# Optimization experiments

Measured on AMD Instinct MI355X. Metric: run time of the kernel, lower is better.

## Reference

```python
import jax, jax.numpy as jnp
import numpy as np
import math

B, S, D, H = 8, 1024, 1024, 16
DK = D // H
DFF = 4 * D
EPS = 1e-5


def gelu_tanh(x):
    # matches the hand-written GELU: 0.5*x*(1+tanh(sqrt(2/pi)*(x+0.044715*x^3)))
    c = math.sqrt(2.0 / math.pi)
    return 0.5 * x * (1.0 + jnp.tanh(c * (x + 0.044715 * x ** 3)))


def layernorm(x, g, b):
    # faithful to the custom LayerNorm: unbiased std (ddof=1), eps added to std
    mean = jnp.mean(x, -1, keepdims=True)
    std = jnp.std(x, -1, keepdims=True, ddof=1)
    return g * (x - mean) / (std + EPS) + b


def setup_inputs() -> dict:
    key = jax.random.key(0)
    ks = jax.random.split(key, 12)
    sc_d = 1.0 / math.sqrt(D)
    sc_f = 1.0 / math.sqrt(DFF)
    inp = {
        "x": jax.random.normal(ks[0], (B, S, D), jnp.float32),
        "mask": jax.random.randint(ks[1], (B, 1, S, S), 0, 2, jnp.int32),
        "wq": jax.random.normal(ks[2], (D, D), jnp.float32) * sc_d,
        "bq": jnp.zeros((D,), jnp.float32),
        "wk": jax.random.normal(ks[3], (D, D), jnp.float32) * sc_d,
        "bk": jnp.zeros((D,), jnp.float32),
        "wv": jax.random.normal(ks[4], (D, D), jnp.float32) * sc_d,
        "bv": jnp.zeros((D,), jnp.float32),
        "wo": jax.random.normal(ks[5], (D, D), jnp.float32) * sc_d,
        "bo": jnp.zeros((D,), jnp.float32),
        "w1": jax.random.normal(ks[6], (DFF, D), jnp.float32) * sc_d,
        "b1": jnp.zeros((DFF,), jnp.float32),
        "w2": jax.random.normal(ks[7], (D, DFF), jnp.float32) * sc_f,
        "b2": jnp.zeros((D,), jnp.float32),
        "ln1_g": jnp.ones((D,), jnp.float32),
        "ln1_b": jnp.zeros((D,), jnp.float32),
        "ln2_g": jnp.ones((D,), jnp.float32),
        "ln2_b": jnp.zeros((D,), jnp.float32),
    }
    return inp


def _mha(xn, mask, wq, bq, wk, bk, wv, bv, wo, bo):
    def proj(w, b):
        y = xn @ w.T + b                       # [B,S,D]
        return y.reshape(B, S, H, DK).transpose(0, 2, 1, 3)  # [B,H,S,DK]
    q, k, v = proj(wq, bq), proj(wk, bk), proj(wv, bv)
    scores = jnp.einsum("bhqd,bhkd->bhqk", q, k) / math.sqrt(DK)
    scores = jnp.where(mask == 0, -1e9, scores)
    p = jax.nn.softmax(scores, axis=-1)
    o = jnp.einsum("bhqk,bhkd->bhqd", p, v)    # [B,H,S,DK]
    o = o.transpose(0, 2, 1, 3).reshape(B, S, D)
    return o @ wo.T + bo


def reference(x, mask, wq, bq, wk, bk, wv, bv, wo, bo, w1, b1, w2, b2,
              ln1_g, ln1_b, ln2_g, ln2_b):
    # dropout is identity in eval mode
    xn = layernorm(x, ln1_g, ln1_b)
    x = x + _mha(xn, mask, wq, bq, wk, bk, wv, bv, wo, bo)
    xn = layernorm(x, ln2_g, ln2_b)
    ff = gelu_tanh(xn @ w1.T + b1) @ w2.T + b2
    return x + ff
```

## Files before the change

kernel.cpp:

```cpp
#include <hip/hip_runtime.h>
#include <stdint.h>

typedef float f32x4 __attribute__((ext_vector_type(4)));
typedef short short8 __attribute__((ext_vector_type(8)));
typedef __bf16 bf16x8 __attribute__((ext_vector_type(8)));

static __device__ __forceinline__ short f2bf(float f) {
  unsigned u = __builtin_bit_cast(unsigned, f);
  u = (u + 0x7FFFu + ((u >> 16) & 1u)) >> 16;
  return (short)u;
}

static __device__ __forceinline__ float bf2f(short s) {
  return __builtin_bit_cast(float, (unsigned)((unsigned short)s) << 16);
}

static __device__ __forceinline__ unsigned pack2bf(float a, float b) {
  return ((unsigned)(unsigned short)f2bf(a)) |
         (((unsigned)(unsigned short)f2bf(b)) << 16);
}

static __device__ __forceinline__ f32x4 mfma16(short8 a, short8 b, f32x4 c) {
  return __builtin_amdgcn_mfma_f32_16x16x32_bf16(
      __builtin_bit_cast(bf16x8, a), __builtin_bit_cast(bf16x8, b), c, 0, 0, 0);
}

static __device__ __forceinline__ void gld_lds16(const void* g, void* s) {
  __builtin_amdgcn_global_load_lds(
      (const __attribute__((address_space(1))) void*)g,
      (__attribute__((address_space(3))) void*)s, 16, 0, 0);
}

__global__ __launch_bounds__(256) void cvt_f2bf(const float* __restrict__ in,
                                                short* __restrict__ out, int n4) {
  int i = blockIdx.x * 256 + threadIdx.x;
  if (i < n4) {
    float4 v = ((const float4*)in)[i];
    short4 o;
    o.x = f2bf(v.x); o.y = f2bf(v.y); o.z = f2bf(v.z); o.w = f2bf(v.w);
    ((short4*)out)[i] = o;
  }
}

__global__ __launch_bounds__(256) void concat3(const float* __restrict__ a,
                                               const float* __restrict__ b,
                                               const float* __restrict__ c,
                                               float* __restrict__ o) {
  int i = blockIdx.x * 256 + threadIdx.x;
  float v = (i < 1024) ? a[i] : ((i < 2048) ? b[i - 1024] : c[i - 2048]);
  o[i] = v;
}

__global__ __launch_bounds__(256) void packmask(const int* __restrict__ m,
                                                unsigned* __restrict__ out) {
  int w = blockIdx.x * 256 + threadIdx.x;
  const int4* p = (const int4*)(m + (size_t)w * 32);
  unsigned bits = 0;
#pragma unroll
  for (int c = 0; c < 8; c++) {
    int4 v = p[c];
    bits |= (unsigned)(v.x != 0) << (c * 4 + 0);
    bits |= (unsigned)(v.y != 0) << (c * 4 + 1);
    bits |= (unsigned)(v.z != 0) << (c * 4 + 2);
    bits |= (unsigned)(v.w != 0) << (c * 4 + 3);
  }
  out[w] = bits;
}

__global__ __launch_bounds__(256) void ln_bf16(const float* __restrict__ x,
                                               const float* __restrict__ g,
                                               const float* __restrict__ bb,
                                               short* __restrict__ out) {
  const int row = blockIdx.x, tid = threadIdx.x;
  const float4 xv = *(const float4*)&x[(size_t)row * 1024 + tid * 4];
  float s = xv.x + xv.y + xv.z + xv.w;
#pragma unroll
  for (int o = 32; o; o >>= 1) s += __shfl_down(s, o);
  __shared__ float red[8];
  if ((tid & 63) == 0) red[tid >> 6] = s;
  __syncthreads();
  const float mean = (red[0] + red[1] + red[2] + red[3]) * (1.f / 1024.f);
  const float a0 = xv.x - mean, a1 = xv.y - mean, a2 = xv.z - mean, a3 = xv.w - mean;
  float ss = a0 * a0 + a1 * a1 + a2 * a2 + a3 * a3;
#pragma unroll
  for (int o = 32; o; o >>= 1) ss += __shfl_down(ss, o);
  if ((tid & 63) == 0) red[4 + (tid >> 6)] = ss;
  __syncthreads();
  const float inv =
      1.f / (sqrtf((red[4] + red[5] + red[6] + red[7]) * (1.f / 1023.f)) + 1e-5f);
  const float4 gv = *(const float4*)&g[tid * 4];
  const float4 bv = *(const float4*)&bb[tid * 4];
  short4 o4;
  o4.x = f2bf(gv.x * a0 * inv + bv.x);
  o4.y = f2bf(gv.y * a1 * inv + bv.y);
  o4.z = f2bf(gv.z * a2 * inv + bv.z);
  o4.w = f2bf(gv.w * a3 * inv + bv.w);
  *(short4*)&out[(size_t)row * 1024 + tid * 4] = o4;
}

template <int ACT, int RES, int OBF>
__global__ __launch_bounds__(256) void gemm_bt(
    const short* __restrict__ A, const short* __restrict__ Bw,
    const float* __restrict__ bias, const float* __restrict__ resid,
    void* __restrict__ Cout, int M, int N, int K) {
  __shared__ alignas(1024) short As[128 * 32];
  __shared__ alignas(1024) short Bs[128 * 32];
  const int tid = threadIdx.x;
  const int l = tid & 63, w = tid >> 6;
  const int wr = w >> 1, wc = w & 1;
  const int m0 = blockIdx.y * 128, n0 = blockIdx.x * 128;
  const int fr = l & 15, fq = l >> 4;
  const size_t Ksz = (size_t)K;

  const short* ag = A + (size_t)(m0 + w * 32 + (l >> 2)) * Ksz + (l & 3) * 8;
  const short* bg = Bw + (size_t)(n0 + w * 32 + (l >> 2)) * Ksz + (l & 3) * 8;
  short* asw = As + w * 1024;
  short* bsw = Bs + w * 1024;

  f32x4 acc[4][4] = {};

  for (int kt = 0; kt < K; kt += 32) {
    gld_lds16(ag + kt, asw);
    gld_lds16(ag + kt + 16 * Ksz, asw + 512);
    gld_lds16(bg + kt, bsw);
    gld_lds16(bg + kt + 16 * Ksz, bsw + 512);
    __syncthreads();
    short8 af[4], bf[4];
#pragma unroll
    for (int m = 0; m < 4; m++)
      af[m] = *(const short8*)&As[(wr * 64 + m * 16 + fr) * 32 + fq * 8];
#pragma unroll
    for (int n = 0; n < 4; n++)
      bf[n] = *(const short8*)&Bs[(wc * 64 + n * 16 + fr) * 32 + fq * 8];
#pragma unroll
    for (int m = 0; m < 4; m++)
#pragma unroll
      for (int n = 0; n < 4; n++) acc[m][n] = mfma16(af[m], bf[n], acc[m][n]);
    __syncthreads();
  }

#pragma unroll
  for (int m = 0; m < 4; m++) {
#pragma unroll
    for (int n = 0; n < 4; n++) {
      const int row = m0 + wr * 64 + m * 16 + fq * 4;
      const int col = n0 + wc * 64 + n * 16 + fr;
      const float bvl = bias[col];
#pragma unroll
      for (int r = 0; r < 4; r++) {
        float v = acc[m][n][r] + bvl;
        if (ACT == 1) {
          float zz = 0.7978845608028654f * (v + 0.044715f * v * v * v);
          float th = 1.f - 2.f / (__expf(2.f * zz) + 1.f);
          v = 0.5f * v * (1.f + th);
        }
        if (RES) v += resid[(size_t)(row + r) * N + col];
        if (OBF)
          ((short*)Cout)[(size_t)(row + r) * N + col] = f2bf(v);
        else
          ((float*)Cout)[(size_t)(row + r) * N + col] = v;
      }
    }
  }
}

__global__ __launch_bounds__(256, 4) void attn_fwd(
    const short* __restrict__ QKV, const unsigned* __restrict__ MW,
    short* __restrict__ Om) {
  const int orig = blockIdx.x;
  const int gid = (orig & 7) * 256 + (orig >> 3);
  const int qt = gid & 15;
  const int h = (gid >> 4) & 15;
  const int b = gid >> 8;
  const int tid = threadIdx.x, l = tid & 63, w = tid >> 6;
  const int fr = l & 15, fq = l >> 4;
  __shared__ alignas(1024) short Ks[2][64 * 64];
  __shared__ alignas(1024) short Vt[2][64 * 64];
  __shared__ alignas(1024) short Ps[4][16 * 64];
  const int qbase = qt * 64;
  const size_t RS = 3072;

  short8 qf0, qf1;
  {
    const short* qp =
        QKV + ((size_t)(b * 1024 + qbase + w * 16 + fr)) * RS + h * 64 + fq * 8;
    qf0 = *(const short8*)qp;
    qf1 = *(const short8*)(qp + 32);
#pragma unroll
    for (int e = 0; e < 8; e++) {
      qf0[e] = f2bf(0.125f * bf2f(qf0[e]));
      qf1[e] = f2bf(0.125f * bf2f(qf1[e]));
    }
  }
  f32x4 m2 = {-1e30f, -1e30f, -1e30f, -1e30f};
  f32x4 lsum = {};
  f32x4 oacc[4] = {};

  const int kcol = (l & 7) ^ ((l >> 3) & 7);
  const short* kg =
      QKV + ((size_t)(b * 1024 + w * 16 + (l >> 3))) * RS + 1024 + h * 64 + kcol * 8;
  const int vkey = w * 16 + (l >> 2), vd0 = (l & 3) * 16;
  const short* vg = QKV + ((size_t)(b * 1024 + vkey)) * RS + 2048 + h * 64 + vd0;
  const int keyp = ((vkey >= 32) ? 32 : 0) + (l >> 2) * 2 + (w & 1);
  const int kslot = keyp >> 3, kbyte = keyp & 7;
  const int vxk = (l & 3) << 1;
  const unsigned* mwp = MW + ((size_t)(b * 1024 + qbase + w * 16 + fq * 4)) * 32;

  gld_lds16(kg, &Ks[0][w * 1024]);
  gld_lds16(kg + 8 * RS, &Ks[0][w * 1024 + 512]);
  short8 vv0 = *(const short8*)vg;
  short8 vv1 = *(const short8*)(vg + 8);
#pragma unroll
  for (int e = 0; e < 8; e++)
    Vt[0][(vd0 + e) * 64 + ((kslot ^ (e & 7) ^ vxk) << 3) + kbyte] = vv0[e];
#pragma unroll
  for (int e = 0; e < 8; e++)
    Vt[0][(vd0 + 8 + e) * 64 + ((kslot ^ (e & 7) ^ vxk) << 3) + kbyte] = vv1[e];
  __syncthreads();

  for (int t = 0; t < 16; t++) {
    const int cur = t & 1;
    if (t < 15) {
      const short* kgn = kg + (size_t)(t + 1) * 64 * RS;
      gld_lds16(kgn, &Ks[cur ^ 1][w * 1024]);
      gld_lds16(kgn + 8 * RS, &Ks[cur ^ 1][w * 1024 + 512]);
      const short* vgn = vg + (size_t)(t + 1) * 64 * RS;
      vv0 = *(const short8*)vgn;
      vv1 = *(const short8*)(vgn + 8);
    }
    f32x4 sv[4];
    __builtin_amdgcn_s_setprio(1);
#pragma unroll
    for (int j = 0; j < 4; j++) {
      const int row = j * 16 + fr;
      short8 k0 = *(const short8*)&Ks[cur][row * 64 + ((fq ^ (fr & 7)) << 3)];
      short8 k1 = *(const short8*)&Ks[cur][row * 64 + (((4 + fq) ^ (fr & 7)) << 3)];
      f32x4 z = {0.f, 0.f, 0.f, 0.f};
      sv[j] = mfma16(qf0, k0, z);
      sv[j] = mfma16(qf1, k1, sv[j]);
    }
    __builtin_amdgcn_s_setprio(0);
#pragma unroll
    for (int r = 0; r < 4; r++) {
      const uint2 mw = *(const uint2*)(mwp + (size_t)r * 32 + t * 2);
      float t0 = ((mw.x >> fr) & 1u) ? sv[0][r] : -3e38f;
      float t1 = ((mw.x >> (16 + fr)) & 1u) ? sv[1][r] : -3e38f;
      float t2 = ((mw.y >> fr) & 1u) ? sv[2][r] : -3e38f;
      float t3 = ((mw.y >> (16 + fr)) & 1u) ? sv[3][r] : -3e38f;
      const float pmax = fmaxf(fmaxf(t0, t1), fmaxf(t2, t3));
      if (!__all(pmax <= m2[r] + 8.f)) {
        float mx = pmax;
        mx = fmaxf(mx, __shfl_xor(mx, 1));
        mx = fmaxf(mx, __shfl_xor(mx, 2));
        mx = fmaxf(mx, __shfl_xor(mx, 4));
        mx = fmaxf(mx, __shfl_xor(mx, 8));
        const float nm = fmaxf(m2[r], mx);
        const float al = __expf(m2[r] - nm);
        m2[r] = nm;
        lsum[r] *= al;
#pragma unroll
        for (int dt = 0; dt < 4; dt++) oacc[dt][r] *= al;
      }
      const float p0 = __expf(t0 - m2[r]);
      const float p1 = __expf(t1 - m2[r]);
      const float p2 = __expf(t2 - m2[r]);
      const float p3 = __expf(t3 - m2[r]);
      lsum[r] += (p0 + p1) + (p2 + p3);
      const int q = fq * 4 + r;
      const int s0 = (fr >> 2) ^ (q & 7);
      const int s1 = (4 + (fr >> 2)) ^ (q & 7);
      *(unsigned*)&Ps[w][q * 64 + (s0 << 3) + ((fr & 3) << 1)] = pack2bf(p0, p1);
      *(unsigned*)&Ps[w][q * 64 + (s1 << 3) + ((fr & 3) << 1)] = pack2bf(p2, p3);
    }
    short8 pa0 = *(const short8*)&Ps[w][fr * 64 + ((fq ^ (fr & 7)) << 3)];
    short8 pa1 = *(const short8*)&Ps[w][fr * 64 + (((4 + fq) ^ (fr & 7)) << 3)];
    __builtin_amdgcn_s_setprio(1);
#pragma unroll
    for (int dt = 0; dt < 4; dt++) {
      const int row = dt * 16 + fr;
      const int vkx = dt << 1;
      short8 v0 = *(const short8*)&Vt[cur][row * 64 + ((fq ^ (fr & 7) ^ vkx) << 3)];
      short8 v1 =
          *(const short8*)&Vt[cur][row * 64 + (((4 + fq) ^ (fr & 7) ^ vkx) << 3)];
      oacc[dt] = mfma16(pa0, v0, oacc[dt]);
      oacc[dt] = mfma16(pa1, v1, oacc[dt]);
    }
    __builtin_amdgcn_s_setprio(0);
    if (t < 15) {
#pragma unroll
      for (int e = 0; e < 8; e++)
        Vt[cur ^ 1][(vd0 + e) * 64 + ((kslot ^ (e & 7) ^ vxk) << 3) + kbyte] = vv0[e];
#pragma unroll
      for (int e = 0; e < 8; e++)
        Vt[cur ^ 1][(vd0 + 8 + e) * 64 + ((kslot ^ (e & 7) ^ vxk) << 3) + kbyte] =
            vv1[e];
    }
    __syncthreads();
  }

#pragma unroll
  for (int r = 0; r < 4; r++) {
    float s = lsum[r];
    s += __shfl_xor(s, 1);
    s += __shfl_xor(s, 2);
    s += __shfl_xor(s, 4);
    s += __shfl_xor(s, 8);
    lsum[r] = s;
  }

#pragma unroll
  for (int dt = 0; dt < 4; dt++) {
#pragma unroll
    for (int r = 0; r < 4; r++) {
      const size_t qrow = (size_t)b * 1024 + qbase + w * 16 + fq * 4 + r;
      Om[qrow * 1024 + h * 64 + dt * 16 + fr] = f2bf(oacc[dt][r] / lsum[r]);
    }
  }
}

extern "C" void kernel_launch(void* const* d_in, const int* in_sizes, int n_in,
                              void* d_out, int out_size, void* d_ws, size_t ws_size,
                              hipStream_t stream) {
  (void)in_sizes; (void)n_in; (void)out_size; (void)ws_size;
  const float* x   = (const float*)d_in[0];
  const int*   msk = (const int*)d_in[1];
  const float* wq  = (const float*)d_in[2];
  const float* bq  = (const float*)d_in[3];
  const float* wk  = (const float*)d_in[4];
  const float* bk  = (const float*)d_in[5];
  const float* wv  = (const float*)d_in[6];
  const float* bv  = (const float*)d_in[7];
  const float* wo  = (const float*)d_in[8];
  const float* bo  = (const float*)d_in[9];
  const float* w1  = (const float*)d_in[10];
  const float* b1  = (const float*)d_in[11];
  const float* w2  = (const float*)d_in[12];
  const float* b2  = (const float*)d_in[13];
  const float* g1  = (const float*)d_in[14];
  const float* be1 = (const float*)d_in[15];
  const float* g2  = (const float*)d_in[16];
  const float* be2 = (const float*)d_in[17];
  float* out = (float*)d_out;

  char* p = (char*)d_ws;
  auto take = [&](size_t n) { char* r = p; p += (n + 1023) & ~(size_t)1023; return r; };
  const size_t MD = (size_t)8192 * 1024;
  short* XN  = (short*)take(MD * 2);
  short* BIG = (short*)take((size_t)8192 * 4096 * 2);
  short* QKV = BIG;
  short* F1  = BIG;
  short* AO  = (short*)take(MD * 2);
  float* X1  = (float*)take(MD * 4);
  unsigned* MW = (unsigned*)take((size_t)8 * 1024 * 32 * 4);
  short* WQKV = (short*)take((size_t)3072 * 1024 * 2);
  short* WO  = (short*)take((size_t)1024 * 1024 * 2);
  short* W1  = (short*)take((size_t)4096 * 1024 * 2);
  short* W2  = (short*)take((size_t)1024 * 4096 * 2);
  float* BQKV = (float*)take((size_t)3072 * 4);

  cvt_f2bf<<<1024, 256, 0, stream>>>(wq, WQKV, 262144);
  cvt_f2bf<<<1024, 256, 0, stream>>>(wk, WQKV + (size_t)1024 * 1024, 262144);
  cvt_f2bf<<<1024, 256, 0, stream>>>(wv, WQKV + (size_t)2048 * 1024, 262144);
  cvt_f2bf<<<1024, 256, 0, stream>>>(wo, WO, 262144);
  cvt_f2bf<<<4096, 256, 0, stream>>>(w1, W1, 1048576);
  cvt_f2bf<<<4096, 256, 0, stream>>>(w2, W2, 1048576);
  concat3<<<12, 256, 0, stream>>>(bq, bk, bv, BQKV);
  packmask<<<1024, 256, 0, stream>>>(msk, MW);
  ln_bf16<<<8192, 256, 0, stream>>>(x, g1, be1, XN);
  gemm_bt<0, 0, 1><<<dim3(24, 64), 256, 0, stream>>>(XN, WQKV, BQKV, nullptr, QKV,
                                                     8192, 3072, 1024);
  attn_fwd<<<2048, 256, 0, stream>>>(QKV, MW, AO);
  gemm_bt<0, 1, 0><<<dim3(8, 64), 256, 0, stream>>>(AO, WO, bo, x, X1, 8192, 1024, 1024);
  ln_bf16<<<8192, 256, 0, stream>>>(X1, g2, be2, XN);
  gemm_bt<1, 0, 1><<<dim3(32, 64), 256, 0, stream>>>(XN, W1, b1, nullptr, F1,
                                                     8192, 4096, 1024);
  gemm_bt<0, 1, 0><<<dim3(8, 64), 256, 0, stream>>>(F1, W2, b2, X1, out,
                                                    8192, 1024, 4096);
}
```

Before: 615.3 us.

## Replace GEMM with 256x256-tile, 8-wave, double-buffered swizzled-LDS pipelined kernel

Replaces the 128x128, single-buffered GEMM with a 256x256-tile kernel using 512 threads and 128KB of dynamic LDS. The kernel double-buffers 64-wide K slices, interleaving async global-to-LDS loads with MFMA quarters under explicit barriers and vmcnt waits. It also XOR-swizzles the LDS layout to avoid bank conflicts, raises MFMA wave priority, and remaps block IDs for L2 locality. This targets the load-latency stalls and low arithmetic intensity of the old GEMM, at the cost of fewer blocks (e.g. 128 for the N=1024 GEMMs) and heavy reliance on hand-tuned barrier placement.

```diff
diff --git a/kernel.cpp b/kernel.cpp
--- a/kernel.cpp
+++ b/kernel.cpp
@@ -30,6 +30,10 @@
       (const __attribute__((address_space(1))) void*)g,
       (__attribute__((address_space(3))) void*)s, 16, 0, 0);
 }
+
+#define BAR() asm volatile("s_barrier" ::: "memory")
+#define VMW6() asm volatile("s_waitcnt vmcnt(6)" ::: "memory")
+#define VMW0() asm volatile("s_waitcnt vmcnt(0)" ::: "memory")
 
 __global__ __launch_bounds__(256) void cvt_f2bf(const float* __restrict__ in,
                                                 short* __restrict__ out, int n4) {
@@ -98,52 +102,125 @@
   *(short4*)&out[(size_t)row * 1024 + tid * 4] = o4;
 }
 
+template <int MH>
+static __device__ __forceinline__ void lda(short8 (&Af)[4][2], const short* As_,
+                                           int fr, int fq) {
+#pragma unroll
+  for (int mm = 0; mm < 4; mm++)
+#pragma unroll
+    for (int kk = 0; kk < 2; kk++)
+      Af[mm][kk] = *(const short8*)&As_[(MH * 64 + mm * 16 + fr) * 64 +
+                                        (((kk * 4 + fq) ^ (fr & 7)) << 3)];
+}
+
+template <int NH>
+static __device__ __forceinline__ void ldb(short8 (&Bf)[2][2], const short* Bs_,
+                                           int brow0, int fr, int fq) {
+#pragma unroll
+  for (int nn = 0; nn < 2; nn++)
+#pragma unroll
+    for (int kk = 0; kk < 2; kk++)
+      Bf[nn][kk] = *(const short8*)&Bs_[(brow0 + NH * 32 + nn * 16 + fr) * 64 +
+                                        (((kk * 4 + fq) ^ (fr & 7)) << 3)];
+}
+
+template <int MH, int NH>
+static __device__ __forceinline__ void mq(f32x4 (&acc)[8][4],
+                                          const short8 (&Af)[4][2],
+                                          const short8 (&Bf)[2][2]) {
+  __builtin_amdgcn_s_setprio(1);
+#pragma unroll
+  for (int mm = 0; mm < 4; mm++)
+#pragma unroll
+    for (int nn = 0; nn < 2; nn++)
+#pragma unroll
+      for (int kk = 0; kk < 2; kk++)
+        acc[MH * 4 + mm][NH * 2 + nn] =
+            mfma16(Af[mm][kk], Bf[nn][kk], acc[MH * 4 + mm][NH * 2 + nn]);
+  __builtin_amdgcn_s_setprio(0);
+}
+
 template <int ACT, int RES, int OBF>
-__global__ __launch_bounds__(256) void gemm_bt(
+__global__ __launch_bounds__(512, 2) void gemm256(
     const short* __restrict__ A, const short* __restrict__ Bw,
     const float* __restrict__ bias, const float* __restrict__ resid,
     void* __restrict__ Cout, int M, int N, int K) {
-  __shared__ alignas(1024) short As[128 * 32];
-  __shared__ alignas(1024) short Bs[128 * 32];
+  extern __shared__ short smem[];
   const int tid = threadIdx.x;
   const int l = tid & 63, w = tid >> 6;
-  const int wr = w >> 1, wc = w & 1;
-  const int m0 = blockIdx.y * 128, n0 = blockIdx.x * 128;
+  const int wr = w >> 2, wc = w & 3;
   const int fr = l & 15, fq = l >> 4;
+  const int gx = gridDim.x;
+  int flat = blockIdx.y * gx + blockIdx.x;
+  {
+    const int chunk = (gx * gridDim.y) >> 3;
+    flat = (flat & 7) * chunk + (flat >> 3);
+  }
+  const int m0 = (flat / gx) * 256, n0 = (flat % gx) * 256;
   const size_t Ksz = (size_t)K;
-
-  const short* ag = A + (size_t)(m0 + w * 32 + (l >> 2)) * Ksz + (l & 3) * 8;
-  const short* bg = Bw + (size_t)(n0 + w * 32 + (l >> 2)) * Ksz + (l & 3) * 8;
-  short* asw = As + w * 1024;
-  short* bsw = Bs + w * 1024;
-
-  f32x4 acc[4][4] = {};
-
-  for (int kt = 0; kt < K; kt += 32) {
-    gld_lds16(ag + kt, asw);
-    gld_lds16(ag + kt + 16 * Ksz, asw + 512);
-    gld_lds16(bg + kt, bsw);
-    gld_lds16(bg + kt + 16 * Ksz, bsw + 512);
-    __syncthreads();
-    short8 af[4], bf[4];
-#pragma unroll
-    for (int m = 0; m < 4; m++)
-      af[m] = *(const short8*)&As[(wr * 64 + m * 16 + fr) * 32 + fq * 8];
-#pragma unroll
-    for (int n = 0; n < 4; n++)
-      bf[n] = *(const short8*)&Bs[(wc * 64 + n * 16 + fr) * 32 + fq * 8];
-#pragma unroll
-    for (int m = 0; m < 4; m++)
-#pragma unroll
-      for (int n = 0; n < 4; n++) acc[m][n] = mfma16(af[m], bf[n], acc[m][n]);
-    __syncthreads();
-  }
-
-#pragma unroll
-  for (int m = 0; m < 4; m++) {
+  const int NT = K >> 6;
+  const int srow = tid >> 3;
+  const int gsw = ((tid & 7) ^ (srow & 7)) << 3;
+  const int brow0 = (wc & 1) * 64;
+
+  auto stage = [&](int bufi, int ab, int h, int s) {
+    const short* gp = (ab ? Bw : A) +
+                      (size_t)((ab ? n0 : m0) + h * 128 + srow) * Ksz + s * 64 + gsw;
+    short* lp = smem + ((((bufi << 1) | ab) << 1) | h) * 8192 + w * 512;
+    gld_lds16(gp, lp);
+    gld_lds16(gp + (size_t)64 * Ksz, lp + 4096);
+  };
+
+  f32x4 acc[8][4] = {};
+  short8 Af[4][2], Bf0[2][2], Bf1[2][2];
+
+  stage(0, 0, 0, 0); stage(0, 0, 1, 0); stage(0, 1, 0, 0); stage(0, 1, 1, 0);
+  stage(1, 1, 0, 1); stage(1, 1, 1, 1); stage(1, 0, 0, 1);
+  VMW6();
+  BAR();
+
+  const short* As_;
+  const short* Bs_;
+  for (int t = 0; t < (NT >> 1); t++) {
+    const int j1 = 2 * t + 1;
+    int s0 = 2 * t + 2; if (s0 >= NT) s0 = NT - 2;
+    int s1 = 2 * t + 3; if (s1 >= NT) s1 = NT - 1;
+
+    As_ = smem + (0 * 4 + 0 * 2 + wr) * 8192;
+    Bs_ = smem + (0 * 4 + 1 * 2 + (wc >> 1)) * 8192;
+    lda<0>(Af, As_, fr, fq); ldb<0>(Bf0, Bs_, brow0, fr, fq);
+    stage(1, 0, 1, j1);
+    BAR(); mq<0, 0>(acc, Af, Bf0); BAR();
+    ldb<1>(Bf1, Bs_, brow0, fr, fq);
+    BAR(); mq<0, 1>(acc, Af, Bf1); BAR();
+    lda<1>(Af, As_, fr, fq);
+    stage(0, 1, 0, s0);
+    BAR(); mq<1, 1>(acc, Af, Bf1); BAR();
+    stage(0, 1, 1, s0); stage(0, 0, 0, s0);
+    VMW6();
+    BAR(); mq<1, 0>(acc, Af, Bf0); BAR();
+
+    As_ = smem + (1 * 4 + 0 * 2 + wr) * 8192;
+    Bs_ = smem + (1 * 4 + 1 * 2 + (wc >> 1)) * 8192;
+    lda<0>(Af, As_, fr, fq); ldb<0>(Bf0, Bs_, brow0, fr, fq);
+    stage(0, 0, 1, s0);
+    BAR(); mq<0, 0>(acc, Af, Bf0); BAR();
+    ldb<1>(Bf1, Bs_, brow0, fr, fq);
+    BAR(); mq<0, 1>(acc, Af, Bf1); BAR();
+    lda<1>(Af, As_, fr, fq);
+    stage(1, 1, 0, s1);
+    BAR(); mq<1, 1>(acc, Af, Bf1); BAR();
+    stage(1, 1, 1, s1); stage(1, 0, 0, s1);
+    VMW6();
+    BAR(); mq<1, 0>(acc, Af, Bf0); BAR();
+  }
+  VMW0();
+
+#pragma unroll
+  for (int m = 0; m < 8; m++) {
 #pragma unroll
     for (int n = 0; n < 4; n++) {
-      const int row = m0 + wr * 64 + m * 16 + fq * 4;
+      const int row = m0 + wr * 128 + m * 16 + fq * 4;
       const int col = n0 + wc * 64 + n * 16 + fr;
       const float bvl = bias[col];
 #pragma unroll
@@ -358,6 +435,14 @@
   short* W2  = (short*)take((size_t)1024 * 4096 * 2);
   float* BQKV = (float*)take((size_t)3072 * 4);
 
+  const int SMEM = 131072;
+  hipFuncSetAttribute((const void*)gemm256<0, 0, 1>,
+                      hipFuncAttributeMaxDynamicSharedMemorySize, SMEM);
+  hipFuncSetAttribute((const void*)gemm256<0, 1, 0>,
+                      hipFuncAttributeMaxDynamicSharedMemorySize, SMEM);
+  hipFuncSetAttribute((const void*)gemm256<1, 0, 1>,
+                      hipFuncAttributeMaxDynamicSharedMemorySize, SMEM);
+
   cvt_f2bf<<<1024, 256, 0, stream>>>(wq, WQKV, 262144);
   cvt_f2bf<<<1024, 256, 0, stream>>>(wk, WQKV + (size_t)1024 * 1024, 262144);
   cvt_f2bf<<<1024, 256, 0, stream>>>(wv, WQKV + (size_t)2048 * 1024, 262144);
@@ -367,13 +452,14 @@
   concat3<<<12, 256, 0, stream>>>(bq, bk, bv, BQKV);
   packmask<<<1024, 256, 0, stream>>>(msk, MW);
   ln_bf16<<<8192, 256, 0, stream>>>(x, g1, be1, XN);
-  gemm_bt<0, 0, 1><<<dim3(24, 64), 256, 0, stream>>>(XN, WQKV, BQKV, nullptr, QKV,
-                                                     8192, 3072, 1024);
+  gemm256<0, 0, 1><<<dim3(12, 32), 512, SMEM, stream>>>(XN, WQKV, BQKV, nullptr,
+                                                        QKV, 8192, 3072, 1024);
   attn_fwd<<<2048, 256, 0, stream>>>(QKV, MW, AO);
-  gemm_bt<0, 1, 0><<<dim3(8, 64), 256, 0, stream>>>(AO, WO, bo, x, X1, 8192, 1024, 1024);
+  gemm256<0, 1, 0><<<dim3(4, 32), 512, SMEM, stream>>>(AO, WO, bo, x, X1, 8192,
+                                                       1024, 1024);
   ln_bf16<<<8192, 256, 0, stream>>>(X1, g2, be2, XN);
-  gemm_bt<1, 0, 1><<<dim3(32, 64), 256, 0, stream>>>(XN, W1, b1, nullptr, F1,
-                                                     8192, 4096, 1024);
-  gemm_bt<0, 1, 0><<<dim3(8, 64), 256, 0, stream>>>(F1, W2, b2, X1, out,
-                                                    8192, 1024, 4096);
-}
+  gemm256<1, 0, 1><<<dim3(16, 32), 512, SMEM, stream>>>(XN, W1, b1, nullptr, F1,
+                                                        8192, 4096, 1024);
+  gemm256<0, 1, 0><<<dim3(4, 32), 512, SMEM, stream>>>(F1, W2, b2, X1, out, 8192,
+                                                       1024, 4096);
+}
```

After: 581.9 us. 1.06x faster.
